# Kernel tuning notes

Hardware: AMD Instinct MI355X
Metric: run time of the kernel (lower is better)

The kernel has to match this reference:

```python
import jax, jax.numpy as jnp
import numpy as np

B, S, D, H, FF = 4, 2048, 1024, 16, 4096
DT, TARGET, ITERS = 0.1, 0.0, 5


def _ln(x, w, b):
    mu = jnp.mean(x, axis=-1, keepdims=True)
    var = jnp.mean((x - mu) ** 2, axis=-1, keepdims=True)
    return (x - mu) * jax.lax.rsqrt(var + 1e-5) * w + b


def setup_inputs() -> dict:
    key = jax.random.key(0)
    ks = iter(jax.random.split(key, 16))
    w = lambda shape: jax.random.normal(next(ks), shape, dtype=jnp.float32) * 0.02
    return {
        "x": jax.random.normal(next(ks), (B, S, D), dtype=jnp.float32),
        "ln_attn_w": jnp.ones((D,), jnp.float32), "ln_attn_b": jnp.zeros((D,), jnp.float32),
        "attn_in_w": w((3 * D, D)), "attn_in_b": jnp.zeros((3 * D,), jnp.float32),
        "attn_out_w": w((D, D)), "attn_out_b": jnp.zeros((D,), jnp.float32),
        "ln1_w": jnp.ones((D,), jnp.float32), "ln1_b": jnp.zeros((D,), jnp.float32),
        "ln2_w": jnp.ones((D,), jnp.float32), "ln2_b": jnp.zeros((D,), jnp.float32),
        "inl_u_w": w((D, D)), "inl_u_b": jnp.zeros((D,), jnp.float32),
        "inl_a_w": w((D, D)), "inl_a_b": jnp.zeros((D,), jnp.float32),
        "inl_b_w": w((D, D)), "inl_b_b": jnp.zeros((D,), jnp.float32),
        "inl_g_w": w((D, D)), "inl_g_b": jnp.zeros((D,), jnp.float32),
        "ff1_w": w((FF, D)), "ff1_b": jnp.zeros((FF,), jnp.float32),
        "ff2_w": w((D, FF)), "ff2_b": jnp.zeros((D,), jnp.float32),
    }


def reference(x, ln_attn_w, ln_attn_b, attn_in_w, attn_in_b, attn_out_w, attn_out_b,
              ln1_w, ln1_b, ln2_w, ln2_b,
              inl_u_w, inl_u_b, inl_a_w, inl_a_b, inl_b_w, inl_b_b, inl_g_w, inl_g_b,
              ff1_w, ff1_b, ff2_w, ff2_b):
    dh = D // H
    scale = 1.0 / np.sqrt(dh).astype(np.float32)
    # --- causal multi-head attention (dropout = identity, eval mode) ---
    xn = _ln(x, ln_attn_w, ln_attn_b)
    qkv = xn @ attn_in_w.T + attn_in_b            # [B,S,3D]
    q, k, v = jnp.split(qkv, 3, axis=-1)
    hsplit = lambda t: t.reshape(B, S, H, dh).transpose(0, 2, 1, 3)  # [B,H,S,dh]
    q, k, v = hsplit(q), hsplit(k), hsplit(v)
    scores = jnp.einsum('bhqd,bhkd->bhqk', q, k) * scale
    causal = jnp.triu(jnp.ones((S, S), dtype=bool), 1)
    scores = jnp.where(causal, jnp.finfo(scores.dtype).min, scores)
    probs = jax.nn.softmax(scores, axis=-1)
    attn_out = jnp.einsum('bhqk,bhkd->bhqd', probs, v).transpose(0, 2, 1, 3).reshape(B, S, D)
    attn_out = attn_out @ attn_out_w.T + attn_out_b
    x = x + attn_out
    context = attn_out
    # --- INL integrator dynamics (controllers depend only on context) ---
    xs = _ln(x, ln1_w, ln1_b)
    vs = jnp.zeros_like(xs)
    u = context @ inl_u_w.T + inl_u_b
    alpha = jax.nn.sigmoid(context @ inl_a_w.T + inl_a_b)
    beta = jax.nn.softplus(context @ inl_b_w.T + inl_b_b)
    g = jax.nn.sigmoid(context @ inl_g_w.T + inl_g_b)
    for _ in range(ITERS):
        vs = vs + DT * (alpha * (TARGET - xs) - beta * vs + u)
        xs = xs + DT * g * vs
    x = x + xs
    # --- feed-forward (exact GELU as torch default) ---
    h = _ln(x, ln2_w, ln2_b)
    x = x + (jax.nn.gelu(h @ ff1_w.T + ff1_b, approximate=False) @ ff2_w.T + ff2_b)
    return x
```

## Files before the change

kernel.cpp:

```cpp
#include <hip/hip_runtime.h>
#include <cstdint>
#include <cmath>

typedef __attribute__((ext_vector_type(4))) float floatx4;
typedef __attribute__((ext_vector_type(8))) __bf16 bf16x8;
typedef __attribute__((ext_vector_type(4))) unsigned short ushort4v;

#define DEVI static __device__ __forceinline__

DEVI unsigned short f2b(float f) {
    unsigned x = __float_as_uint(f);
    return (unsigned short)((x + 0x7fffu + ((x >> 16) & 1u)) >> 16);
}
DEVI float b2f(unsigned short u) { return __uint_as_float(((unsigned)u) << 16); }

DEVI void load16(void* lds, const void* g) {
    __builtin_amdgcn_global_load_lds(
        (__attribute__((address_space(1))) void*)(const_cast<void*>(g)),
        (__attribute__((address_space(3))) void*)lds, 16, 0, 0);
}

DEVI floatx4 MFMA16(bf16x8 a, bf16x8 b, floatx4 c) {
    return __builtin_amdgcn_mfma_f32_16x16x32_bf16(a, b, c, 0, 0, 0);
}

__global__ __launch_bounds__(256) void cvt_kernel(const float* __restrict__ src,
                                                  unsigned short* __restrict__ dst, int n4) {
    int i = blockIdx.x * 256 + threadIdx.x;
    if (i >= n4) return;
    floatx4 v = ((const floatx4*)src)[i];
    ushort4v o;
    o[0] = f2b(v[0]); o[1] = f2b(v[1]); o[2] = f2b(v[2]); o[3] = f2b(v[3]);
    ((ushort4v*)dst)[i] = o;
}

__global__ __launch_bounds__(256) void catbias_kernel(const float* __restrict__ a,
                                                      const float* __restrict__ b,
                                                      const float* __restrict__ c,
                                                      const float* __restrict__ d,
                                                      float* __restrict__ o) {
    int i = blockIdx.x * 256 + threadIdx.x;
    int p = i >> 10, j = i & 1023;
    float v = (p == 0) ? a[j] : (p == 1) ? b[j] : (p == 2) ? c[j] : d[j];
    o[i] = v;
}

__global__ __launch_bounds__(256) void ln_kernel(const float* __restrict__ in,
                                                 const float* __restrict__ w,
                                                 const float* __restrict__ b,
                                                 unsigned short* __restrict__ obf,
                                                 float* __restrict__ of) {
    const int row = blockIdx.x, tid = threadIdx.x;
    const floatx4* pr = (const floatx4*)(in + (size_t)row * 1024);
    floatx4 v = pr[tid];
    float s  = v[0] + v[1] + v[2] + v[3];
    float ss = v[0]*v[0] + v[1]*v[1] + v[2]*v[2] + v[3]*v[3];
    #pragma unroll
    for (int o = 32; o >= 1; o >>= 1) { s += __shfl_xor(s, o); ss += __shfl_xor(ss, o); }
    __shared__ float red[8];
    int wv = tid >> 6, lane = tid & 63;
    if (lane == 0) { red[wv] = s; red[4 + wv] = ss; }
    __syncthreads();
    s  = red[0] + red[1] + red[2] + red[3];
    ss = red[4] + red[5] + red[6] + red[7];
    float mu  = s * (1.0f / 1024.0f);
    float var = ss * (1.0f / 1024.0f) - mu * mu;
    float rstd = rsqrtf(var + 1e-5f);
    floatx4 wv4 = ((const floatx4*)w)[tid];
    floatx4 bv4 = ((const floatx4*)b)[tid];
    floatx4 o;
    #pragma unroll
    for (int c = 0; c < 4; c++) o[c] = (v[c] - mu) * rstd * wv4[c] + bv4[c];
    if (obf) {
        ushort4v t;
        t[0] = f2b(o[0]); t[1] = f2b(o[1]); t[2] = f2b(o[2]); t[3] = f2b(o[3]);
        ((ushort4v*)(obf + (size_t)row * 1024))[tid] = t;
    }
    if (of) ((floatx4*)(of + (size_t)row * 1024))[tid] = o;
}

__global__ __launch_bounds__(256) void integrator_kernel(const float* __restrict__ xs0,
                                                         const unsigned short* __restrict__ uabg,
                                                         float* __restrict__ xio) {
    size_t i = (size_t)blockIdx.x * 256 + threadIdx.x;
    size_t tok = i >> 8;
    int grp = (int)(i & 255) * 4;
    const unsigned short* ubase = uabg + tok * 4096 + grp;
    ushort4v uu = *(const ushort4v*)(ubase);
    ushort4v aa = *(const ushort4v*)(ubase + 1024);
    ushort4v bb = *(const ushort4v*)(ubase + 2048);
    ushort4v gg = *(const ushort4v*)(ubase + 3072);
    floatx4 xsv = ((const floatx4*)xs0)[i];
    floatx4 x1  = ((const floatx4*)xio)[i];
    floatx4 res;
    #pragma unroll
    for (int c = 0; c < 4; c++) {
        float u = b2f(uu[c]), a = b2f(aa[c]), bt = b2f(bb[c]), g = b2f(gg[c]);
        float xs = xsv[c], vs = 0.f;
        #pragma unroll
        for (int t = 0; t < 5; t++) {
            vs += 0.1f * (-a * xs - bt * vs + u);
            xs += 0.1f * g * vs;
        }
        res[c] = x1[c] + xs;
    }
    ((floatx4*)xio)[i] = res;
}

template <int EPI>
__global__ __launch_bounds__(256, 4) void gemm_bt(const unsigned short* __restrict__ A,
                                                  const unsigned short* __restrict__ W,
                                                  const float* __restrict__ bias, int K,
                                                  unsigned short* __restrict__ ob0,
                                                  unsigned short* __restrict__ ob1,
                                                  unsigned short* __restrict__ ob2,
                                                  float* __restrict__ of0,
                                                  const float* __restrict__ xres) {
    __shared__ unsigned short sA[2][128 * 32];
    __shared__ unsigned short sB[2][128 * 32];
    const int tid = threadIdx.x;
    const int wave = tid >> 6, lane = tid & 63;
    const int ln = lane & 15, quad = lane >> 4;
    const int gx = gridDim.x;
    const int flat = blockIdx.y * gx + blockIdx.x;
    const int cpx = (gx * (int)gridDim.y) >> 3;
    const int rmp = (flat & 7) * cpx + (flat >> 3);
    const size_t m0 = (size_t)(rmp / gx) * 128;
    const int n0 = (rmp % gx) * 128;
    const int wm = (wave >> 1) * 64, wn = (wave & 1) * 64;

    const floatx4 z4 = {0.f, 0.f, 0.f, 0.f};
    floatx4 acc[4][4];
    #pragma unroll
    for (int mt = 0; mt < 4; mt++)
        #pragma unroll
        for (int nt = 0; nt < 4; nt++) acc[mt][nt] = z4;

    const int r16 = lane >> 2;
    const int gsw = (((lane & 3) ^ (r16 & 3) ^ ((r16 >> 2) & 3))) * 8;
    const int arow = wave * 16 + r16;
    const unsigned short* gA = A + (m0 + (size_t)arow) * K + gsw;
    const unsigned short* gB = W + ((size_t)(n0 + arow)) * K + gsw;
    const size_t rs64 = (size_t)64 * K;
    const int so = wave * 512;
    const int swr = ((quad ^ (ln & 3) ^ ((ln >> 2) & 3))) * 8;

    const int T = K >> 5;

    load16(&sA[0][so], gA);
    load16(&sA[0][so + 2048], gA + rs64);
    load16(&sB[0][so], gB);
    load16(&sB[0][so + 2048], gB + rs64);
    asm volatile("s_waitcnt vmcnt(0)" ::: "memory");
    asm volatile("s_barrier" ::: "memory");

    #pragma unroll 1
    for (int t = 0; t < T; t++) {
        const int c = t & 1;
        if (t + 1 < T) {
            const int k = (t + 1) * 32;
            load16(&sA[c ^ 1][so], gA + k);
            load16(&sA[c ^ 1][so + 2048], gA + rs64 + k);
            load16(&sB[c ^ 1][so], gB + k);
            load16(&sB[c ^ 1][so + 2048], gB + rs64 + k);
        }
        __builtin_amdgcn_sched_barrier(0);
        bf16x8 fa[4], fb[4];
        #pragma unroll
        for (int mt = 0; mt < 4; mt++)
            fa[mt] = *(const bf16x8*)&sA[c][(wm + mt * 16 + ln) * 32 + swr];
        #pragma unroll
        for (int nt = 0; nt < 4; nt++)
            fb[nt] = *(const bf16x8*)&sB[c][(wn + nt * 16 + ln) * 32 + swr];
        asm volatile("s_waitcnt lgkmcnt(0)" ::: "memory");
        __builtin_amdgcn_sched_barrier(0);
        __builtin_amdgcn_s_setprio(1);
        #pragma unroll
        for (int mt = 0; mt < 4; mt++)
            #pragma unroll
            for (int nt = 0; nt < 4; nt++)
                acc[mt][nt] = MFMA16(fa[mt], fb[nt], acc[mt][nt]);
        __builtin_amdgcn_s_setprio(0);
        __builtin_amdgcn_sched_barrier(0);
        if (t + 1 < T) {
            asm volatile("s_waitcnt vmcnt(0)" ::: "memory");
            asm volatile("s_barrier" ::: "memory");
        }
    }

    const size_t rowb = m0 + wm + quad * 4;
    const int colb = n0 + wn + ln;
    #pragma unroll
    for (int mt = 0; mt < 4; mt++) {
        #pragma unroll
        for (int nt = 0; nt < 4; nt++) {
            const int n = colb + nt * 16;
            const float bs = bias[n];
            #pragma unroll
            for (int r = 0; r < 4; r++) {
                const size_t row = rowb + mt * 16 + r;
                float c = acc[mt][nt][r] + bs;
                if constexpr (EPI == 0) {
                    int sect = n >> 10, d1 = n & 1023, h = d1 >> 6, d = d1 & 63;
                    int bb = (int)(row >> 11), s = (int)(row & 2047);
                    size_t bh = (size_t)(bb * 16 + h);
                    if (sect == 0)      ob0[(bh * 2048 + s) * 64 + d] = f2b(c);
                    else if (sect == 1) ob1[(bh * 2048 + s) * 64 + d] = f2b(c);
                    else                ob2[(bh * 64 + d) * 2048 + s] = f2b(c);
                } else if constexpr (EPI == 1) {
                    size_t idx = row * 1024 + n;
                    ob0[idx] = f2b(c);
                    of0[idx] = xres[idx] + c;
                } else if constexpr (EPI == 2) {
                    int p = n >> 10;
                    float v;
                    if (p == 0)       v = c;
                    else if (p == 2)  v = fmaxf(c, 0.f) + log1pf(__expf(-fabsf(c)));
                    else              v = 1.f / (1.f + __expf(-c));
                    ob0[row * 4096 + n] = f2b(v);
                } else if constexpr (EPI == 3) {
                    float v = 0.5f * c * (1.f + erff(c * 0.70710678118654752f));
                    ob0[row * 4096 + n] = f2b(v);
                } else {
                    size_t idx = row * 1024 + n;
                    of0[idx] += c;
                }
            }
        }
    }
}

#define PSTR 72
__global__ __launch_bounds__(256, 3) void attn_kernel(const unsigned short* __restrict__ Qb,
                                                      const unsigned short* __restrict__ Kb,
                                                      const unsigned short* __restrict__ Vtb,
                                                      unsigned short* __restrict__ Ob) {
    __shared__ unsigned short sK[2][64 * 64];
    __shared__ unsigned short sVt[2][64 * 64];
    __shared__ unsigned short sQP[128 * PSTR];
    const int pr = blockIdx.x;
    const int bh = blockIdx.y;
    const int tid = threadIdx.x, wave = tid >> 6, lane = tid & 63;
    const int ln = lane & 15, quad = lane >> 4;
    const unsigned short* Q  = Qb  + (size_t)bh * 2048 * 64;
    const unsigned short* Kp = Kb  + (size_t)bh * 2048 * 64;
    const unsigned short* Vt = Vtb + (size_t)bh * 64 * 2048;

    const int rl  = lane >> 3;
    const int gsw = (((lane & 7) ^ rl)) * 8;
    const int sseg = wave * 2;
    const unsigned short* kbase = Kp + (size_t)(sseg * 8 + rl) * 64 + gsw;
    const unsigned short* vbase = Vt + (size_t)(sseg * 8 + rl) * 2048 + gsw;
    unsigned short* sP = &sQP[wave * 32 * PSTR];
    const int bb = bh >> 4, h = bh & 15;
    const floatx4 z4 = {0.f, 0.f, 0.f, 0.f};

    #pragma unroll 1
    for (int phase = 0; phase < 2; phase++) {
        const int qt = phase ? pr : (15 - pr);
        const int q0 = qt * 128;
        const int T = 2 * qt + 2;

        #pragma unroll
        for (int i = 0; i < 4; i++) {
            int s = wave * 4 + i;
            load16(&sQP[s * 512], Q + (size_t)(q0 + s * 8 + rl) * 64 + gsw);
        }
        load16(&sK[0][sseg * 512], kbase);
        load16(&sK[0][(sseg + 1) * 512], kbase + (size_t)8 * 64);
        load16(&sVt[0][sseg * 512], vbase);
        load16(&sVt[0][(sseg + 1) * 512], vbase + (size_t)8 * 2048);
        asm volatile("s_waitcnt vmcnt(0)" ::: "memory");
        asm volatile("s_barrier" ::: "memory");

        bf16x8 aq[2][2];
        #pragma unroll
        for (int mt = 0; mt < 2; mt++)
            #pragma unroll
            for (int ks = 0; ks < 2; ks++)
                aq[mt][ks] = *(const bf16x8*)&sQP[(wave * 32 + mt * 16 + ln) * 64 +
                                                  (((ks * 4 + quad) ^ (ln & 7)) * 8)];
        asm volatile("s_waitcnt lgkmcnt(0)" ::: "memory");
        asm volatile("s_barrier" ::: "memory");

        floatx4 Oacc[2][4];
        float m_run[2][4], l_run[2][4];
        #pragma unroll
        for (int mt = 0; mt < 2; mt++)
            #pragma unroll
            for (int j = 0; j < 4; j++) { Oacc[mt][j] = z4; m_run[mt][j] = -1e30f; l_run[mt][j] = 0.f; }

        const int wave_first = q0 + wave * 32;
        const int wave_last  = wave_first + 31;

        #pragma unroll 1
        for (int t = 0; t < T; t++) {
            const int kk0 = t * 64;
            const int cur = t & 1;
            if (t + 1 < T) {
                const unsigned short* kg = kbase + (size_t)(kk0 + 64) * 64;
                const unsigned short* vg = vbase + (size_t)(kk0 + 64);
                load16(&sK[cur ^ 1][sseg * 512], kg);
                load16(&sK[cur ^ 1][(sseg + 1) * 512], kg + (size_t)8 * 64);
                load16(&sVt[cur ^ 1][sseg * 512], vg);
                load16(&sVt[cur ^ 1][(sseg + 1) * 512], vg + (size_t)8 * 2048);
                asm volatile("s_waitcnt vmcnt(4)" ::: "memory");
            } else {
                asm volatile("s_waitcnt vmcnt(0)" ::: "memory");
            }
            asm volatile("s_barrier" ::: "memory");

            if (kk0 <= wave_last) {
                floatx4 Sc[2][4];
                #pragma unroll
                for (int mt = 0; mt < 2; mt++)
                    #pragma unroll
                    for (int nt = 0; nt < 4; nt++) Sc[mt][nt] = z4;
                __builtin_amdgcn_s_setprio(1);
                #pragma unroll
                for (int ks = 0; ks < 2; ks++) {
                    #pragma unroll
                    for (int nt = 0; nt < 4; nt++) {
                        bf16x8 bk = *(const bf16x8*)&sK[cur][(nt * 16 + ln) * 64 +
                                                             (((ks * 4 + quad) ^ (ln & 7)) * 8)];
                        #pragma unroll
                        for (int mt = 0; mt < 2; mt++)
                            Sc[mt][nt] = MFMA16(aq[mt][ks], bk, Sc[mt][nt]);
                    }
                }
                __builtin_amdgcn_s_setprio(0);
                const bool diag = (kk0 + 63 > wave_first);
                #pragma unroll
                for (int mt = 0; mt < 2; mt++)
                    #pragma unroll
                    for (int nt = 0; nt < 4; nt++)
                        #pragma unroll
                        for (int r = 0; r < 4; r++) {
                            float v = Sc[mt][nt][r] * 0.125f;
                            if (diag) {
                                int rowg = wave_first + mt * 16 + quad * 4 + r;
                                int colg = kk0 + nt * 16 + ln;
                                if (colg > rowg) v = -1e30f;
                            }
                            Sc[mt][nt][r] = v;
                        }
                float alpha[2][4];
                #pragma unroll
                for (int mt = 0; mt < 2; mt++)
                    #pragma unroll
                    for (int r = 0; r < 4; r++) {
                        float mx = fmaxf(fmaxf(Sc[mt][0][r], Sc[mt][1][r]), fmaxf(Sc[mt][2][r], Sc[mt][3][r]));
                        #pragma unroll
                        for (int off = 1; off < 16; off <<= 1) mx = fmaxf(mx, __shfl_xor(mx, off));
                        float mnew = fmaxf(m_run[mt][r], mx);
                        alpha[mt][r] = __expf(m_run[mt][r] - mnew);
                        m_run[mt][r] = mnew;
                    }
                #pragma unroll
                for (int mt = 0; mt < 2; mt++)
                    #pragma unroll
                    for (int r = 0; r < 4; r++) {
                        float rs = 0.f;
                        #pragma unroll
                        for (int nt = 0; nt < 4; nt++) {
                            float p = __expf(Sc[mt][nt][r] - m_run[mt][r]);
                            Sc[mt][nt][r] = p;
                            rs += p;
                        }
                        #pragma unroll
                        for (int off = 1; off < 16; off <<= 1) rs += __shfl_xor(rs, off);
                        l_run[mt][r] = l_run[mt][r] * alpha[mt][r] + rs;
                    }
                #pragma unroll
                for (int mt = 0; mt < 2; mt++)
                    #pragma unroll
                    for (int nt = 0; nt < 4; nt++)
                        #pragma unroll
                        for (int r = 0; r < 4; r++) Oacc[mt][nt][r] *= alpha[mt][r];
                #pragma unroll
                for (int mt = 0; mt < 2; mt++)
                    #pragma unroll
                    for (int nt = 0; nt < 4; nt++)
                        #pragma unroll
                        for (int r = 0; r < 4; r++)
                            sP[(mt * 16 + quad * 4 + r) * PSTR + nt * 16 + ln] = f2b(Sc[mt][nt][r]);
                __builtin_amdgcn_s_setprio(1);
                #pragma unroll
                for (int kp = 0; kp < 2; kp++) {
                    bf16x8 ap[2];
                    #pragma unroll
                    for (int mt = 0; mt < 2; mt++)
                        ap[mt] = *(const bf16x8*)&sP[(mt * 16 + ln) * PSTR + kp * 32 + quad * 8];
                    #pragma unroll
                    for (int nt = 0; nt < 4; nt++) {
                        bf16x8 bv = *(const bf16x8*)&sVt[cur][(nt * 16 + ln) * 64 +
                                                              (((kp * 4 + quad) ^ (ln & 7)) * 8)];
                        #pragma unroll
                        for (int mt = 0; mt < 2; mt++)
                            Oacc[mt][nt] = MFMA16(ap[mt], bv, Oacc[mt][nt]);
                    }
                }
                __builtin_amdgcn_s_setprio(0);
            }
            asm volatile("s_barrier" ::: "memory");
        }

        #pragma unroll
        for (int mt = 0; mt < 2; mt++)
            #pragma unroll
            for (int nt = 0; nt < 4; nt++)
                #pragma unroll
                for (int r = 0; r < 4; r++) {
                    float o = Oacc[mt][nt][r] / l_run[mt][r];
                    int srow = q0 + wave * 32 + mt * 16 + quad * 4 + r;
                    size_t tok = (size_t)bb * 2048 + srow;
                    Ob[tok * 1024 + h * 64 + nt * 16 + ln] = f2b(o);
                }
    }
}

extern "C" void kernel_launch(void* const* d_in, const int* in_sizes, int n_in,
                              void* d_out, int out_size, void* d_ws, size_t ws_size,
                              hipStream_t stream) {
    const float* x          = (const float*)d_in[0];
    const float* ln_attn_w  = (const float*)d_in[1];
    const float* ln_attn_b  = (const float*)d_in[2];
    const float* attn_in_w  = (const float*)d_in[3];
    const float* attn_in_b  = (const float*)d_in[4];
    const float* attn_out_w = (const float*)d_in[5];
    const float* attn_out_b = (const float*)d_in[6];
    const float* ln1_w      = (const float*)d_in[7];
    const float* ln1_b      = (const float*)d_in[8];
    const float* ln2_w      = (const float*)d_in[9];
    const float* ln2_b      = (const float*)d_in[10];
    const float* inl_u_w    = (const float*)d_in[11];
    const float* inl_u_b    = (const float*)d_in[12];
    const float* inl_a_w    = (const float*)d_in[13];
    const float* inl_a_b    = (const float*)d_in[14];
    const float* inl_b_w    = (const float*)d_in[15];
    const float* inl_b_b    = (const float*)d_in[16];
    const float* inl_g_w    = (const float*)d_in[17];
    const float* inl_g_b    = (const float*)d_in[18];
    const float* ff1_w      = (const float*)d_in[19];
    const float* ff1_b      = (const float*)d_in[20];
    const float* ff2_w      = (const float*)d_in[21];
    const float* ff2_b      = (const float*)d_in[22];
    float* out = (float*)d_out;

    char* ws = (char*)d_ws;
    unsigned short* Wqkv  = (unsigned short*)(ws);
    unsigned short* Wout  = (unsigned short*)(ws + 6291456);
    unsigned short* Winl  = (unsigned short*)(ws + 8388608);
    unsigned short* Wff1  = (unsigned short*)(ws + 16777216);
    unsigned short* Wff2  = (unsigned short*)(ws + 25165824);
    unsigned short* xnb   = (unsigned short*)(ws + 33554432);
    unsigned short* qb    = (unsigned short*)(ws + 50331648);
    unsigned short* kb    = (unsigned short*)(ws + 67108864);
    unsigned short* vtb   = (unsigned short*)(ws + 83886080);
    unsigned short* attnb = (unsigned short*)(ws + 100663296);
    unsigned short* ctxb  = (unsigned short*)(ws + 117440512);
    float*          xs    = (float*)(ws + 134217728);
    float*          bias4 = (float*)(ws + 167772160);
    unsigned short* uabg  = (unsigned short*)(ws + 50331648);
    unsigned short* ff1b  = (unsigned short*)(ws + 50331648);

    cvt_kernel<<<3072, 256, 0, stream>>>(attn_in_w, Wqkv, 786432);
    cvt_kernel<<<1024, 256, 0, stream>>>(attn_out_w, Wout, 262144);
    cvt_kernel<<<1024, 256, 0, stream>>>(inl_u_w, Winl + 0, 262144);
    cvt_kernel<<<1024, 256, 0, stream>>>(inl_a_w, Winl + 1048576, 262144);
    cvt_kernel<<<1024, 256, 0, stream>>>(inl_b_w, Winl + 2097152, 262144);
    cvt_kernel<<<1024, 256, 0, stream>>>(inl_g_w, Winl + 3145728, 262144);
    cvt_kernel<<<4096, 256, 0, stream>>>(ff1_w, Wff1, 1048576);
    cvt_kernel<<<4096, 256, 0, stream>>>(ff2_w, Wff2, 1048576);
    catbias_kernel<<<16, 256, 0, stream>>>(inl_u_b, inl_a_b, inl_b_b, inl_g_b, bias4);

    ln_kernel<<<8192, 256, 0, stream>>>(x, ln_attn_w, ln_attn_b, xnb, nullptr);
    gemm_bt<0><<<dim3(24, 64), 256, 0, stream>>>(xnb, Wqkv, attn_in_b, 1024, qb, kb, vtb, nullptr, nullptr);
    attn_kernel<<<dim3(8, 64), 256, 0, stream>>>(qb, kb, vtb, attnb);
    gemm_bt<1><<<dim3(8, 64), 256, 0, stream>>>(attnb, Wout, attn_out_b, 1024, ctxb, nullptr, nullptr, out, x);
    ln_kernel<<<8192, 256, 0, stream>>>(out, ln1_w, ln1_b, nullptr, xs);
    gemm_bt<2><<<dim3(32, 64), 256, 0, stream>>>(ctxb, Winl, bias4, 1024, uabg, nullptr, nullptr, nullptr, nullptr);
    integrator_kernel<<<8192, 256, 0, stream>>>(xs, uabg, out);
    ln_kernel<<<8192, 256, 0, stream>>>(out, ln2_w, ln2_b, xnb, nullptr);
    gemm_bt<3><<<dim3(32, 64), 256, 0, stream>>>(xnb, Wff1, ff1_b, 1024, ff1b, nullptr, nullptr, nullptr, nullptr);
    gemm_bt<4><<<dim3(8, 64), 256, 0, stream>>>(ff1b, Wff2, ff2_b, 4096, nullptr, nullptr, nullptr, out, nullptr);
}
```

Baseline: 901.0 us.

## Process two M tiles per GEMM block and overlap epilogue with next prefetch

Each GEMM block now computes two consecutive 128-row tiles sharing the same weight columns, halving the grid. It issues the first k-stage loads of the second tile before running the epilogue of the first, so global loads overlap the epilogue stores. The eight weight-conversion launches are also merged into one kernel to cut launch overhead. Risks: fewer blocks reduce parallelism (e.g. 256 blocks for the N=1024 GEMMs on a 256-CU part), and reusing the same B tile gives no real LDS reuse since B is reloaded each k-loop.

```diff
diff --git a/kernel.cpp b/kernel.cpp
--- a/kernel.cpp
+++ b/kernel.cpp
@@ -24,14 +24,34 @@
     return __builtin_amdgcn_mfma_f32_16x16x32_bf16(a, b, c, 0, 0, 0);
 }
 
-__global__ __launch_bounds__(256) void cvt_kernel(const float* __restrict__ src,
-                                                  unsigned short* __restrict__ dst, int n4) {
+__global__ __launch_bounds__(256) void cvt_all(const float* __restrict__ s0,
+                                               const float* __restrict__ s1,
+                                               const float* __restrict__ s2,
+                                               const float* __restrict__ s3,
+                                               const float* __restrict__ s4,
+                                               const float* __restrict__ s5,
+                                               const float* __restrict__ s6,
+                                               const float* __restrict__ s7,
+                                               unsigned short* d0, unsigned short* d1,
+                                               unsigned short* d2, unsigned short* d3,
+                                               unsigned short* d4, unsigned short* d5,
+                                               unsigned short* d6, unsigned short* d7) {
     int i = blockIdx.x * 256 + threadIdx.x;
-    if (i >= n4) return;
-    floatx4 v = ((const floatx4*)src)[i];
+    int seg = i >> 18;
+    int j = i & 262143;
+    const float* src; unsigned short* dst;
+    if (seg < 3)        { src = s0; dst = d0; j += seg * 262144; }
+    else if (seg == 3)  { src = s1; dst = d1; }
+    else if (seg == 4)  { src = s2; dst = d2; }
+    else if (seg == 5)  { src = s3; dst = d3; }
+    else if (seg == 6)  { src = s4; dst = d4; }
+    else if (seg == 7)  { src = s5; dst = d5; }
+    else if (seg < 12)  { src = s6; dst = d6; j += (seg - 8) * 262144; }
+    else                { src = s7; dst = d7; j += (seg - 12) * 262144; }
+    floatx4 v = ((const floatx4*)src)[j];
     ushort4v o;
     o[0] = f2b(v[0]); o[1] = f2b(v[1]); o[2] = f2b(v[2]); o[3] = f2b(v[3]);
-    ((ushort4v*)dst)[i] = o;
+    ((ushort4v*)dst)[j] = o;
 }
 
 __global__ __launch_bounds__(256) void catbias_kernel(const float* __restrict__ a,
@@ -125,109 +145,125 @@
     const int flat = blockIdx.y * gx + blockIdx.x;
     const int cpx = (gx * (int)gridDim.y) >> 3;
     const int rmp = (flat & 7) * cpx + (flat >> 3);
-    const size_t m0 = (size_t)(rmp / gx) * 128;
+    const size_t m0s = (size_t)(rmp / gx) * 256;
     const int n0 = (rmp % gx) * 128;
     const int wm = (wave >> 1) * 64, wn = (wave & 1) * 64;
 
     const floatx4 z4 = {0.f, 0.f, 0.f, 0.f};
     floatx4 acc[4][4];
-    #pragma unroll
-    for (int mt = 0; mt < 4; mt++)
-        #pragma unroll
-        for (int nt = 0; nt < 4; nt++) acc[mt][nt] = z4;
 
     const int r16 = lane >> 2;
     const int gsw = (((lane & 3) ^ (r16 & 3) ^ ((r16 >> 2) & 3))) * 8;
     const int arow = wave * 16 + r16;
-    const unsigned short* gA = A + (m0 + (size_t)arow) * K + gsw;
-    const unsigned short* gB = W + ((size_t)(n0 + arow)) * K + gsw;
+    const unsigned short* gA0 = A + (m0s + (size_t)arow) * K + gsw;
+    const unsigned short* gA1 = A + (m0s + 128 + (size_t)arow) * K + gsw;
+    const unsigned short* gB  = W + ((size_t)(n0 + arow)) * K + gsw;
     const size_t rs64 = (size_t)64 * K;
     const int so = wave * 512;
     const int swr = ((quad ^ (ln & 3) ^ ((ln >> 2) & 3))) * 8;
 
     const int T = K >> 5;
 
-    load16(&sA[0][so], gA);
-    load16(&sA[0][so + 2048], gA + rs64);
-    load16(&sB[0][so], gB);
-    load16(&sB[0][so + 2048], gB + rs64);
-    asm volatile("s_waitcnt vmcnt(0)" ::: "memory");
-    asm volatile("s_barrier" ::: "memory");
-
-    #pragma unroll 1
-    for (int t = 0; t < T; t++) {
-        const int c = t & 1;
-        if (t + 1 < T) {
-            const int k = (t + 1) * 32;
-            load16(&sA[c ^ 1][so], gA + k);
-            load16(&sA[c ^ 1][so + 2048], gA + rs64 + k);
-            load16(&sB[c ^ 1][so], gB + k);
-            load16(&sB[c ^ 1][so + 2048], gB + rs64 + k);
+    auto stage0 = [&](const unsigned short* gA) {
+        load16(&sA[0][so], gA);
+        load16(&sA[0][so + 2048], gA + rs64);
+        load16(&sB[0][so], gB);
+        load16(&sB[0][so + 2048], gB + rs64);
+    };
+
+    auto kloop = [&](const unsigned short* gA) {
+        #pragma unroll
+        for (int mt = 0; mt < 4; mt++)
+            #pragma unroll
+            for (int nt = 0; nt < 4; nt++) acc[mt][nt] = z4;
+        #pragma unroll 1
+        for (int t = 0; t < T; t++) {
+            const int c = t & 1;
+            if (t + 1 < T) {
+                const int k = (t + 1) * 32;
+                load16(&sA[c ^ 1][so], gA + k);
+                load16(&sA[c ^ 1][so + 2048], gA + rs64 + k);
+                load16(&sB[c ^ 1][so], gB + k);
+                load16(&sB[c ^ 1][so + 2048], gB + rs64 + k);
+            }
+            __builtin_amdgcn_sched_barrier(0);
+            bf16x8 fa[4], fb[4];
+            #pragma unroll
+            for (int mt = 0; mt < 4; mt++)
+                fa[mt] = *(const bf16x8*)&sA[c][(wm + mt * 16 + ln) * 32 + swr];
+            #pragma unroll
+            for (int nt = 0; nt < 4; nt++)
+                fb[nt] = *(const bf16x8*)&sB[c][(wn + nt * 16 + ln) * 32 + swr];
+            asm volatile("s_waitcnt lgkmcnt(0)" ::: "memory");
+            __builtin_amdgcn_sched_barrier(0);
+            __builtin_amdgcn_s_setprio(1);
+            #pragma unroll
+            for (int mt = 0; mt < 4; mt++)
+                #pragma unroll
+                for (int nt = 0; nt < 4; nt++)
+                    acc[mt][nt] = MFMA16(fa[mt], fb[nt], acc[mt][nt]);
+            __builtin_amdgcn_s_setprio(0);
+            __builtin_amdgcn_sched_barrier(0);
+            if (t + 1 < T) {
+                asm volatile("s_waitcnt vmcnt(0)" ::: "memory");
+                asm volatile("s_barrier" ::: "memory");
+            }
         }
-        __builtin_amdgcn_sched_barrier(0);
-        bf16x8 fa[4], fb[4];
-        #pragma unroll
-        for (int mt = 0; mt < 4; mt++)
-            fa[mt] = *(const bf16x8*)&sA[c][(wm + mt * 16 + ln) * 32 + swr];
-        #pragma unroll
-        for (int nt = 0; nt < 4; nt++)
-            fb[nt] = *(const bf16x8*)&sB[c][(wn + nt * 16 + ln) * 32 + swr];
-        asm volatile("s_waitcnt lgkmcnt(0)" ::: "memory");
-        __builtin_amdgcn_sched_barrier(0);
-        __builtin_amdgcn_s_setprio(1);
-        #pragma unroll
-        for (int mt = 0; mt < 4; mt++)
-            #pragma unroll
-            for (int nt = 0; nt < 4; nt++)
-                acc[mt][nt] = MFMA16(fa[mt], fb[nt], acc[mt][nt]);
-        __builtin_amdgcn_s_setprio(0);
-        __builtin_amdgcn_sched_barrier(0);
-        if (t + 1 < T) {
-            asm volatile("s_waitcnt vmcnt(0)" ::: "memory");
-            asm volatile("s_barrier" ::: "memory");
-        }
-    }
-
-    const size_t rowb = m0 + wm + quad * 4;
-    const int colb = n0 + wn + ln;
-    #pragma unroll
-    for (int mt = 0; mt < 4; mt++) {
-        #pragma unroll
-        for (int nt = 0; nt < 4; nt++) {
-            const int n = colb + nt * 16;
-            const float bs = bias[n];
-            #pragma unroll
-            for (int r = 0; r < 4; r++) {
-                const size_t row = rowb + mt * 16 + r;
-                float c = acc[mt][nt][r] + bs;
-                if constexpr (EPI == 0) {
-                    int sect = n >> 10, d1 = n & 1023, h = d1 >> 6, d = d1 & 63;
-                    int bb = (int)(row >> 11), s = (int)(row & 2047);
-                    size_t bh = (size_t)(bb * 16 + h);
-                    if (sect == 0)      ob0[(bh * 2048 + s) * 64 + d] = f2b(c);
-                    else if (sect == 1) ob1[(bh * 2048 + s) * 64 + d] = f2b(c);
-                    else                ob2[(bh * 64 + d) * 2048 + s] = f2b(c);
-                } else if constexpr (EPI == 1) {
-                    size_t idx = row * 1024 + n;
-                    ob0[idx] = f2b(c);
-                    of0[idx] = xres[idx] + c;
-                } else if constexpr (EPI == 2) {
-                    int p = n >> 10;
-                    float v;
-                    if (p == 0)       v = c;
-                    else if (p == 2)  v = fmaxf(c, 0.f) + log1pf(__expf(-fabsf(c)));
-                    else              v = 1.f / (1.f + __expf(-c));
-                    ob0[row * 4096 + n] = f2b(v);
-                } else if constexpr (EPI == 3) {
-                    float v = 0.5f * c * (1.f + erff(c * 0.70710678118654752f));
-                    ob0[row * 4096 + n] = f2b(v);
-                } else {
-                    size_t idx = row * 1024 + n;
-                    of0[idx] += c;
+    };
+
+    auto epilogue = [&](size_t m0b) {
+        const size_t rowb = m0b + wm + quad * 4;
+        const int colb = n0 + wn + ln;
+        #pragma unroll
+        for (int mt = 0; mt < 4; mt++) {
+            #pragma unroll
+            for (int nt = 0; nt < 4; nt++) {
+                const int n = colb + nt * 16;
+                const float bs = bias[n];
+                #pragma unroll
+                for (int r = 0; r < 4; r++) {
+                    const size_t row = rowb + mt * 16 + r;
+                    float c = acc[mt][nt][r] + bs;
+                    if constexpr (EPI == 0) {
+                        int sect = n >> 10, d1 = n & 1023, h = d1 >> 6, d = d1 & 63;
+                        int bb = (int)(row >> 11), s = (int)(row & 2047);
+                        size_t bh = (size_t)(bb * 16 + h);
+                        if (sect == 0)      ob0[(bh * 2048 + s) * 64 + d] = f2b(c);
+                        else if (sect == 1) ob1[(bh * 2048 + s) * 64 + d] = f2b(c);
+                        else                ob2[(bh * 64 + d) * 2048 + s] = f2b(c);
+                    } else if constexpr (EPI == 1) {
+                        size_t idx = row * 1024 + n;
+                        ob0[idx] = f2b(c);
+                        of0[idx] = xres[idx] + c;
+                    } else if constexpr (EPI == 2) {
+                        int p = n >> 10;
+                        float v;
+                        if (p == 0)       v = c;
+                        else if (p == 2)  v = fmaxf(c, 0.f) + log1pf(__expf(-fabsf(c)));
+                        else              v = 1.f / (1.f + __expf(-c));
+                        ob0[row * 4096 + n] = f2b(v);
+                    } else if constexpr (EPI == 3) {
+                        float v = 0.5f * c * (1.f + erff(c * 0.70710678118654752f));
+                        ob0[row * 4096 + n] = f2b(v);
+                    } else {
+                        size_t idx = row * 1024 + n;
+                        of0[idx] += c;
+                    }
                 }
             }
         }
-    }
+    };
+
+    stage0(gA0);
+    asm volatile("s_waitcnt vmcnt(0)" ::: "memory");
+    asm volatile("s_barrier" ::: "memory");
+    kloop(gA0);
+    stage0(gA1);
+    epilogue(m0s);
+    asm volatile("s_waitcnt vmcnt(0)" ::: "memory");
+    asm volatile("s_barrier" ::: "memory");
+    kloop(gA1);
+    epilogue(m0s + 128);
 }
 
 #define PSTR 72
@@ -464,24 +500,20 @@
     unsigned short* uabg  = (unsigned short*)(ws + 50331648);
     unsigned short* ff1b  = (unsigned short*)(ws + 50331648);
 
-    cvt_kernel<<<3072, 256, 0, stream>>>(attn_in_w, Wqkv, 786432);
-    cvt_kernel<<<1024, 256, 0, stream>>>(attn_out_w, Wout, 262144);
-    cvt_kernel<<<1024, 256, 0, stream>>>(inl_u_w, Winl + 0, 262144);
-    cvt_kernel<<<1024, 256, 0, stream>>>(inl_a_w, Winl + 1048576, 262144);
-    cvt_kernel<<<1024, 256, 0, stream>>>(inl_b_w, Winl + 2097152, 262144);
-    cvt_kernel<<<1024, 256, 0, stream>>>(inl_g_w, Winl + 3145728, 262144);
-    cvt_kernel<<<4096, 256, 0, stream>>>(ff1_w, Wff1, 1048576);
-    cvt_kernel<<<4096, 256, 0, stream>>>(ff2_w, Wff2, 1048576);
+    cvt_all<<<16384, 256, 0, stream>>>(attn_in_w, attn_out_w, inl_u_w, inl_a_w,
+                                       inl_b_w, inl_g_w, ff1_w, ff2_w,
+                                       Wqkv, Wout, Winl, Winl + 1048576,
+                                       Winl + 2097152, Winl + 3145728, Wff1, Wff2);
     catbias_kernel<<<16, 256, 0, stream>>>(inl_u_b, inl_a_b, inl_b_b, inl_g_b, bias4);
 
     ln_kernel<<<8192, 256, 0, stream>>>(x, ln_attn_w, ln_attn_b, xnb, nullptr);
-    gemm_bt<0><<<dim3(24, 64), 256, 0, stream>>>(xnb, Wqkv, attn_in_b, 1024, qb, kb, vtb, nullptr, nullptr);
+    gemm_bt<0><<<dim3(24, 32), 256, 0, stream>>>(xnb, Wqkv, attn_in_b, 1024, qb, kb, vtb, nullptr, nullptr);
     attn_kernel<<<dim3(8, 64), 256, 0, stream>>>(qb, kb, vtb, attnb);
-    gemm_bt<1><<<dim3(8, 64), 256, 0, stream>>>(attnb, Wout, attn_out_b, 1024, ctxb, nullptr, nullptr, out, x);
+    gemm_bt<1><<<dim3(8, 32), 256, 0, stream>>>(attnb, Wout, attn_out_b, 1024, ctxb, nullptr, nullptr, out, x);
     ln_kernel<<<8192, 256, 0, stream>>>(out, ln1_w, ln1_b, nullptr, xs);
-    gemm_bt<2><<<dim3(32, 64), 256, 0, stream>>>(ctxb, Winl, bias4, 1024, uabg, nullptr, nullptr, nullptr, nullptr);
+    gemm_bt<2><<<dim3(32, 32), 256, 0, stream>>>(ctxb, Winl, bias4, 1024, uabg, nullptr, nullptr, nullptr, nullptr);
     integrator_kernel<<<8192, 256, 0, stream>>>(xs, uabg, out);
     ln_kernel<<<8192, 256, 0, stream>>>(out, ln2_w, ln2_b, xnb, nullptr);
-    gemm_bt<3><<<dim3(32, 64), 256, 0, stream>>>(xnb, Wff1, ff1_b, 1024, ff1b, nullptr, nullptr, nullptr, nullptr);
-    gemm_bt<4><<<dim3(8, 64), 256, 0, stream>>>(ff1b, Wff2, ff2_b, 4096, nullptr, nullptr, nullptr, out, nullptr);
-}
+    gemm_bt<3><<<dim3(32, 32), 256, 0, stream>>>(xnb, Wff1, ff1_b, 1024, ff1b, nullptr, nullptr, nullptr, nullptr);
+    gemm_bt<4><<<dim3(8, 32), 256, 0, stream>>>(ff1b, Wff2, ff2_b, 4096, nullptr, nullptr, nullptr, out, nullptr);
+}
```

Result: slower. 1.145 ms (+27.1%).
